# Optimization experiments

Measured on AMD Instinct MI355X. Metric: run time of the kernel, lower is better.

## Reference

```python
import jax, jax.numpy as jnp
import numpy as np
from jax import lax

K = 3
BN_EPS = 1e-5


def knn3(x1, x2):
    """x1: (B,N,3), x2: (B,M,3). Returns squared dists (B,N,K) sorted ascending and idx (B,N,K)."""
    # squared euclidean distances via ||a||^2 + ||b||^2 - 2 a.b
    d = (jnp.sum(x1 * x1, -1)[..., :, None]
         + jnp.sum(x2 * x2, -1)[..., None, :]
         - 2.0 * jnp.einsum('bnc,bmc->bnm', x1, x2))  # (B,N,M)
    neg_d, idx = lax.top_k(-d, K)  # smallest distances first
    return -neg_d, idx


def conv_bn_relu(x, W, b, gamma, beta):
    """1x1 Conv1d + BatchNorm1d (training-mode batch stats) + relu. x: (B,C_in,N)."""
    y = jnp.einsum('oc,bcn->bon', W, x) + b[None, :, None]
    mean = jnp.mean(y, axis=(0, 2), keepdims=True)
    var = jnp.mean((y - mean) ** 2, axis=(0, 2), keepdims=True)  # biased, as torch BN
    y = (y - mean) * lax.rsqrt(var + BN_EPS)
    y = y * gamma[None, :, None] + beta[None, :, None]
    return jax.nn.relu(y)


def setup_inputs() -> dict:
    key = jax.random.key(0)
    ks = jax.random.split(key, 12)
    B, N, M = 8, 8192, 2048
    C2, C1 = 256, 128          # points2 / points1 channels
    Cin = C2 + C1              # MLP input after concat
    H1, H2 = 256, 256          # mlp=[256,256]
    inp = {
        'xyz1': jax.random.normal(ks[0], (B, 3, N), jnp.float32),
        'xyz2': jax.random.normal(ks[1], (B, 3, M), jnp.float32),
        'points1': jax.random.normal(ks[2], (B, C1, N), jnp.float32),
        'points2': jax.random.normal(ks[3], (B, C2, M), jnp.float32),
        'W1': jax.random.normal(ks[4], (H1, Cin), jnp.float32) * (1.0 / np.sqrt(Cin)),
        'b1': jax.random.normal(ks[5], (H1,), jnp.float32) * 0.01,
        'g1': jnp.ones((H1,), jnp.float32),
        'beta1': jnp.zeros((H1,), jnp.float32),
        'W2': jax.random.normal(ks[6], (H2, H1), jnp.float32) * (1.0 / np.sqrt(H1)),
        'b2': jax.random.normal(ks[7], (H2,), jnp.float32) * 0.01,
        'g2': jnp.ones((H2,), jnp.float32),
        'beta2': jnp.zeros((H2,), jnp.float32),
    }
    return inp


def reference(xyz1, xyz2, points1, points2, W1, b1, g1, beta1, W2, b2, g2, beta2):
    # (B,3,N)->(B,N,3)
    x1 = jnp.swapaxes(xyz1, -2, -1)
    x2 = jnp.swapaxes(xyz2, -2, -1)
    p2 = jnp.swapaxes(points2, -2, -1)  # (B,M,C2)

    dist, idx = knn3(x1, x2)  # (B,N,K) squared dists, sorted ascending

    # gather neighbor features: (B,N,K,C2)
    nn_points = jax.vmap(lambda p, i: p[i])(p2, idx)

    # inverse-distance weights (faithful: clamp to 1e-10, then 1/(d+1e-8))
    dist = jnp.maximum(dist, 1e-10)
    dist_recip = 1.0 / (dist + 1e-8)
    weight = dist_recip / jnp.sum(dist_recip, axis=-1, keepdims=True)  # (B,N,K)

    interpolated = jnp.einsum('bnkc,bnk->bcn', nn_points, weight)  # (B,C2,N)

    new_points = jnp.concatenate([interpolated, points1], axis=1)  # (B,C2+C1,N)
    new_points = conv_bn_relu(new_points, W1, b1, g1, beta1)
    new_points = conv_bn_relu(new_points, W2, b2, g2, beta2)
    return new_points
```

## Files before the change

kernel.cpp:

```cpp
#include <hip/hip_runtime.h>
#include <cfloat>
#include <cmath>

#define B_    8
#define N_    8192
#define M_    2048
#define C1_   128
#define C2_   256
#define CIN_  384
#define H_    256
#define BNEPS 1e-5f
#define TJ    64
#define NBLK  ((N_ / TJ) * B_)

typedef __bf16 bf16x8 __attribute__((ext_vector_type(8)));
typedef float  f32x4  __attribute__((ext_vector_type(4)));

__device__ __forceinline__ bool lexless(float d, int m, float dk, int ik) {
    return (d < dk) | ((d == dk) & (m < ik));
}
__device__ __forceinline__ void ins3(float d, int m,
                                     float& d0, int& i0, float& d1, int& i1,
                                     float& d2, int& i2) {
    if (lexless(d, m, d2, i2)) {
        if (lexless(d, m, d1, i1)) {
            d2 = d1; i2 = i1;
            if (lexless(d, m, d0, i0)) { d1 = d0; i1 = i0; d0 = d; i0 = m; }
            else                       { d1 = d;  i1 = m; }
        } else { d2 = d; i2 = m; }
    }
}

__global__ __launch_bounds__(256) void knn_kernel(const float* __restrict__ xyz1,
                                                  const float* __restrict__ xyz2,
                                                  float* __restrict__ wsW,
                                                  int* __restrict__ wsI) {
    __shared__ float4 pts[M_];
    const int b = blockIdx.y;
    const int t = threadIdx.x;
    const int n = blockIdx.x * 64 + (t >> 2);
    const int q = t & 3;

    const float* x2 = xyz2 + (size_t)b * 3 * M_;
    for (int m = t; m < M_; m += 256) {
        float x = x2[m], y = x2[M_ + m], z = x2[2 * M_ + m];
        pts[m] = make_float4(x, y, z, fmaf(z, z, fmaf(y, y, x * x)));
    }
    __syncthreads();

    const float* x1 = xyz1 + (size_t)b * 3 * N_;
    const float px = x1[n], py = x1[N_ + n], pz = x1[2 * N_ + n];
    const float s1 = fmaf(pz, pz, fmaf(py, py, px * px));
    const float ax = -2.0f * px, ay = -2.0f * py, az = -2.0f * pz;

    float d0 = FLT_MAX, d1 = FLT_MAX, d2 = FLT_MAX;
    int   i0 = 0x7fffffff, i1 = 0x7fffffff, i2 = 0x7fffffff;

    const float4* p = pts + q;
    #pragma unroll 8
    for (int it = 0; it < M_ / 4; ++it) {
        const float4 pt = p[it * 4];
        const float d = fmaf(ax, pt.x, fmaf(ay, pt.y, fmaf(az, pt.z, s1 + pt.w)));
        const int m = it * 4 + q;
        const bool c0 = d < d0, c1 = d < d1, c2 = d < d2;
        i2 = c1 ? i1 : (c2 ? m : i2);
        i1 = c0 ? i0 : (c1 ? m : i1);
        i0 = c0 ? m  : i0;
        d2 = __builtin_amdgcn_fmed3f(d, d1, d2);
        d1 = __builtin_amdgcn_fmed3f(d, d0, d1);
        d0 = fminf(d, d0);
    }

    #pragma unroll
    for (int delta = 1; delta <= 2; delta <<= 1) {
        float e0 = __shfl_xor(d0, delta), e1 = __shfl_xor(d1, delta), e2 = __shfl_xor(d2, delta);
        int   j0 = __shfl_xor(i0, delta), j1 = __shfl_xor(i1, delta), j2 = __shfl_xor(i2, delta);
        ins3(e0, j0, d0, i0, d1, i1, d2, i2);
        ins3(e1, j1, d0, i0, d1, i1, d2, i2);
        ins3(e2, j2, d0, i0, d1, i1, d2, i2);
    }

    if (q == 0) {
        const float e0 = fmaxf(d0, 1e-10f) + 1e-8f;
        const float e1 = fmaxf(d1, 1e-10f) + 1e-8f;
        const float e2 = fmaxf(d2, 1e-10f) + 1e-8f;
        const float r0 = 1.0f / e0, r1 = 1.0f / e1, r2 = 1.0f / e2;
        const float sum = r0 + r1 + r2;
        const int BNtot = B_ * N_;
        const int base  = b * N_ + n;
        wsW[base] = r0 / sum;  wsW[BNtot + base] = r1 / sum;  wsW[2 * BNtot + base] = r2 / sum;
        wsI[base] = i0;        wsI[BNtot + base] = i1;        wsI[2 * BNtot + base] = i2;
    }
}

__global__ __launch_bounds__(256) void tp2_kernel(const float* __restrict__ p2,
                                                  __bf16* __restrict__ p2t) {
    __shared__ float tile[32][33];
    const int b  = blockIdx.z;
    const int c0 = blockIdx.x * 32, m0 = blockIdx.y * 32;
    const int tx = threadIdx.x & 31, ty = threadIdx.x >> 5;
    const float* src = p2 + ((size_t)b * C2_ + c0) * M_ + m0;
    #pragma unroll
    for (int r = 0; r < 32; r += 8) tile[ty + r][tx] = src[(size_t)(ty + r) * M_ + tx];
    __syncthreads();
    __bf16* dst = p2t + ((size_t)b * M_ + m0) * C2_ + c0;
    #pragma unroll
    for (int r = 0; r < 32; r += 8) dst[(size_t)(ty + r) * C2_ + tx] = (__bf16)tile[tx][ty + r];
}

__global__ __launch_bounds__(256) void packW_kernel(const float* __restrict__ W,
                                                    unsigned short* __restrict__ Wp,
                                                    int Cin) {
    const int tid = blockIdx.x * 256 + threadIdx.x;
    const int total = (Cin / 32) * 16 * 64;
    if (tid >= total) return;
    const int lane = tid & 63;
    const int ob   = (tid >> 6) & 15;
    const int kc   = tid >> 10;
    const int row  = ob * 16 + (lane & 15);
    const int k0   = kc * 32 + (lane >> 4) * 8;
    const float* src = W + (size_t)row * Cin + k0;
    __bf16* dst = (__bf16*)(Wp + (size_t)tid * 8);
    #pragma unroll
    for (int e = 0; e < 8; ++e) dst[e] = (__bf16)src[e];
}

__global__ __launch_bounds__(256, 2) void gemm1_kernel(const float* __restrict__ points1,
                                                       const __bf16* __restrict__ p2t,
                                                       const bf16x8* __restrict__ W1f,
                                                       const float* __restrict__ bias1,
                                                       const float* __restrict__ wsW,
                                                       const int* __restrict__ wsI,
                                                       __bf16* __restrict__ Y1bf,
                                                       float* __restrict__ partS,
                                                       float* __restrict__ partS2) {
    __shared__ __align__(16) unsigned short Bfrag[2][4][64][8];
    __shared__ float wsh[3][TJ];
    __shared__ int   ish[3][TJ];

    const int b  = blockIdx.y;
    const int n0 = blockIdx.x * TJ;
    const int t  = threadIdx.x;
    const int wave = t >> 6, lane = t & 63;
    const int pid  = b * (N_ / TJ) + blockIdx.x;
    const int BNtot = B_ * N_;

    if (t < 3 * TJ) {
        int k = t / TJ, j = t % TJ;
        wsh[k][j] = wsW[k * BNtot + b * N_ + n0 + j];
        ish[k][j] = wsI[k * BNtot + b * N_ + n0 + j];
    }
    __syncthreads();

    const int j = t >> 2, q = t & 3;
    const float w0 = wsh[0][j], w1 = wsh[1][j], w2 = wsh[2][j];
    const __bf16* r0 = p2t + ((size_t)(b * M_ + ish[0][j])) * C2_;
    const __bf16* r1 = p2t + ((size_t)(b * M_ + ish[1][j])) * C2_;
    const __bf16* r2 = p2t + ((size_t)(b * M_ + ish[2][j])) * C2_;
    const float* p1b = points1 + (size_t)b * C1_ * N_ + n0 + j;
    uint4* dstB[2] = { (uint4*)&Bfrag[0][j >> 4][q * 16 + (j & 15)][0],
                       (uint4*)&Bfrag[1][j >> 4][q * 16 + (j & 15)][0] };

    struct Stage { bf16x8 a, b, c; float f[8]; };
    auto issue = [&](int kc, Stage& S) {
        if (kc < C2_ / 32) {
            const int off = kc * 32 + q * 8;
            S.a = *(const bf16x8*)(r0 + off);
            S.b = *(const bf16x8*)(r1 + off);
            S.c = *(const bf16x8*)(r2 + off);
        } else {
            const int cbase = kc * 32 - C2_ + q * 8;
            #pragma unroll
            for (int e = 0; e < 8; ++e) S.f[e] = p1b[(size_t)(cbase + e) * N_];
        }
    };
    auto packwrite = [&](int kc, const Stage& S, uint4* dst) {
        union { __bf16 h[8]; uint4 u4; } pk;
        if (kc < C2_ / 32) {
            #pragma unroll
            for (int e = 0; e < 8; ++e)
                pk.h[e] = (__bf16)fmaf(w2, (float)S.c[e],
                               fmaf(w1, (float)S.b[e], w0 * (float)S.a[e]));
        } else {
            #pragma unroll
            for (int e = 0; e < 8; ++e) pk.h[e] = (__bf16)S.f[e];
        }
        *dst = pk.u4;
    };

    f32x4 acc[4][4];
    #pragma unroll
    for (int rb = 0; rb < 4; ++rb)
        #pragma unroll
        for (int nb = 0; nb < 4; ++nb) acc[rb][nb] = (f32x4){0.f, 0.f, 0.f, 0.f};

    Stage L;
    bf16x8 af[4], afn[4];
    issue(0, L);
    #pragma unroll
    for (int rb = 0; rb < 4; ++rb)
        af[rb] = W1f[((size_t)0 * 16 + wave * 4 + rb) * 64 + lane];
    packwrite(0, L, dstB[0]);
    __syncthreads();

    #pragma unroll
    for (int kc = 0; kc < CIN_ / 32; ++kc) {
        constexpr int NK = CIN_ / 32;
        Stage Ln;
        if (kc + 1 < NK) {
            issue(kc + 1, Ln);
            #pragma unroll
            for (int rb = 0; rb < 4; ++rb)
                afn[rb] = W1f[((size_t)(kc + 1) * 16 + wave * 4 + rb) * 64 + lane];
        }
        bf16x8 bfr[4];
        #pragma unroll
        for (int nb = 0; nb < 4; ++nb)
            bfr[nb] = *reinterpret_cast<const bf16x8*>(&Bfrag[kc & 1][nb][lane][0]);
        #pragma unroll
        for (int rb = 0; rb < 4; ++rb)
            #pragma unroll
            for (int nb = 0; nb < 4; ++nb)
                acc[rb][nb] = __builtin_amdgcn_mfma_f32_16x16x32_bf16(af[rb], bfr[nb],
                                                                      acc[rb][nb], 0, 0, 0);
        if (kc + 1 < NK) {
            packwrite(kc + 1, Ln, dstB[(kc + 1) & 1]);
            #pragma unroll
            for (int rb = 0; rb < 4; ++rb) af[rb] = afn[rb];
        }
        __syncthreads();
    }

    const int rrow = (lane >> 4) * 4, col = lane & 15;
    #pragma unroll
    for (int rb = 0; rb < 4; ++rb) {
        #pragma unroll
        for (int r = 0; r < 4; ++r) {
            const int o = wave * 64 + rb * 16 + rrow + r;
            const float bv = bias1[o];
            float s = 0.f, s2 = 0.f;
            #pragma unroll
            for (int nb = 0; nb < 4; ++nb) {
                float val = acc[rb][nb][r] + bv;
                Y1bf[((size_t)b * H_ + o) * N_ + n0 + nb * 16 + col] = (__bf16)val;
                s += val;
                s2 = fmaf(val, val, s2);
            }
            #pragma unroll
            for (int delta = 1; delta < 16; delta <<= 1) {
                s  += __shfl_xor(s, delta);
                s2 += __shfl_xor(s2, delta);
            }
            if (col == 0) {
                partS [(size_t)o * NBLK + pid] = s;
                partS2[(size_t)o * NBLK + pid] = s2;
            }
        }
    }
}

__global__ __launch_bounds__(256) void reduce_stats(const float* __restrict__ partS,
                                                    const float* __restrict__ partS2,
                                                    const float* __restrict__ g,
                                                    const float* __restrict__ beta,
                                                    float* __restrict__ sc,
                                                    float* __restrict__ sh) {
    const int c = blockIdx.x;
    const int t = threadIdx.x;
    double s = 0.0, s2 = 0.0;
    #pragma unroll
    for (int i = t; i < NBLK; i += 256) {
        s  += (double)partS [(size_t)c * NBLK + i];
        s2 += (double)partS2[(size_t)c * NBLK + i];
    }
    __shared__ double ls[256], ls2[256];
    ls[t] = s; ls2[t] = s2;
    __syncthreads();
    for (int off = 128; off > 0; off >>= 1) {
        if (t < off) { ls[t] += ls[t + off]; ls2[t] += ls2[t + off]; }
        __syncthreads();
    }
    if (t == 0) {
        const double cnt = (double)B_ * N_;
        double mean = ls[0] / cnt;
        double var  = ls2[0] / cnt - mean * mean;
        float rstd  = (float)(1.0 / sqrt(var + (double)BNEPS));
        float scale = rstd * g[c];
        sc[c] = scale;
        sh[c] = beta[c] - (float)mean * scale;
    }
}

__global__ __launch_bounds__(256, 2) void gemm2_kernel(const bf16x8* __restrict__ W2f,
                                                       const float* __restrict__ bias2,
                                                       const float* __restrict__ sc1,
                                                       const float* __restrict__ sh1,
                                                       __bf16* __restrict__ Ybf,
                                                       float* __restrict__ partS,
                                                       float* __restrict__ partS2) {
    __shared__ __align__(16) unsigned short Bfrag[2][4][64][8];
    __shared__ float scs[H_], shs[H_];

    const int b  = blockIdx.y;
    const int n0 = blockIdx.x * TJ;
    const int t  = threadIdx.x;
    const int wave = t >> 6, lane = t & 63;
    const int pid  = b * (N_ / TJ) + blockIdx.x;

    scs[t] = sc1[t];
    shs[t] = sh1[t];
    __syncthreads();

    const int j = t >> 2, q = t & 3;
    __bf16* Yb = Ybf + (size_t)b * H_ * N_;
    const __bf16* src = Yb + n0 + j;
    uint4* dstB[2] = { (uint4*)&Bfrag[0][j >> 4][q * 16 + (j & 15)][0],
                       (uint4*)&Bfrag[1][j >> 4][q * 16 + (j & 15)][0] };

    auto issue = [&](int kc, float L[8]) {
        #pragma unroll
        for (int e = 0; e < 8; ++e)
            L[e] = (float)src[(size_t)(kc * 32 + q * 8 + e) * N_];
    };
    auto packwrite = [&](int kc, const float L[8], uint4* dst) {
        union { __bf16 h[8]; uint4 u4; } pk;
        #pragma unroll
        for (int e = 0; e < 8; ++e) {
            const int c = kc * 32 + q * 8 + e;
            pk.h[e] = (__bf16)fmaxf(fmaf(L[e], scs[c], shs[c]), 0.0f);
        }
        *dst = pk.u4;
    };

    f32x4 acc[4][4];
    #pragma unroll
    for (int rb = 0; rb < 4; ++rb)
        #pragma unroll
        for (int nb = 0; nb < 4; ++nb) acc[rb][nb] = (f32x4){0.f, 0.f, 0.f, 0.f};

    float L[8];
    bf16x8 af[4], afn[4];
    issue(0, L);
    #pragma unroll
    for (int rb = 0; rb < 4; ++rb)
        af[rb] = W2f[((size_t)0 * 16 + wave * 4 + rb) * 64 + lane];
    packwrite(0, L, dstB[0]);
    __syncthreads();

    #pragma unroll
    for (int kc = 0; kc < H_ / 32; ++kc) {
        constexpr int NK = H_ / 32;
        float Ln[8];
        if (kc + 1 < NK) {
            issue(kc + 1, Ln);
            #pragma unroll
            for (int rb = 0; rb < 4; ++rb)
                afn[rb] = W2f[((size_t)(kc + 1) * 16 + wave * 4 + rb) * 64 + lane];
        }
        bf16x8 bfr[4];
        #pragma unroll
        for (int nb = 0; nb < 4; ++nb)
            bfr[nb] = *reinterpret_cast<const bf16x8*>(&Bfrag[kc & 1][nb][lane][0]);
        #pragma unroll
        for (int rb = 0; rb < 4; ++rb)
            #pragma unroll
            for (int nb = 0; nb < 4; ++nb)
                acc[rb][nb] = __builtin_amdgcn_mfma_f32_16x16x32_bf16(af[rb], bfr[nb],
                                                                      acc[rb][nb], 0, 0, 0);
        if (kc + 1 < NK) {
            packwrite(kc + 1, Ln, dstB[(kc + 1) & 1]);
            #pragma unroll
            for (int rb = 0; rb < 4; ++rb) af[rb] = afn[rb];
        }
        __syncthreads();
    }

    const int rrow = (lane >> 4) * 4, col = lane & 15;
    #pragma unroll
    for (int rb = 0; rb < 4; ++rb) {
        #pragma unroll
        for (int r = 0; r < 4; ++r) {
            const int o = wave * 64 + rb * 16 + rrow + r;
            const float bv = bias2[o];
            float s = 0.f, s2 = 0.f;
            #pragma unroll
            for (int nb = 0; nb < 4; ++nb) {
                float val = acc[rb][nb][r] + bv;
                Yb[(size_t)o * N_ + n0 + nb * 16 + col] = (__bf16)val;
                s += val;
                s2 = fmaf(val, val, s2);
            }
            #pragma unroll
            for (int delta = 1; delta < 16; delta <<= 1) {
                s  += __shfl_xor(s, delta);
                s2 += __shfl_xor(s2, delta);
            }
            if (col == 0) {
                partS [(size_t)o * NBLK + pid] = s;
                partS2[(size_t)o * NBLK + pid] = s2;
            }
        }
    }
}

__global__ __launch_bounds__(256) void bnrelu_kernel(const __bf16* __restrict__ Ybf,
                                                     float* __restrict__ out,
                                                     const float* __restrict__ sc,
                                                     const float* __restrict__ sh) {
    const size_t total8 = (size_t)B_ * H_ * N_ / 8;
    const size_t stride = (size_t)gridDim.x * 256;
    for (size_t i = (size_t)blockIdx.x * 256 + threadIdx.x; i < total8; i += stride) {
        bf16x8 v = ((const bf16x8*)Ybf)[i];
        const int c = (int)((i / (N_ / 8)) % H_);
        const float a = sc[c], d = sh[c];
        float4 lo, hi;
        lo.x = fmaxf(fmaf((float)v[0], a, d), 0.f);
        lo.y = fmaxf(fmaf((float)v[1], a, d), 0.f);
        lo.z = fmaxf(fmaf((float)v[2], a, d), 0.f);
        lo.w = fmaxf(fmaf((float)v[3], a, d), 0.f);
        hi.x = fmaxf(fmaf((float)v[4], a, d), 0.f);
        hi.y = fmaxf(fmaf((float)v[5], a, d), 0.f);
        hi.z = fmaxf(fmaf((float)v[6], a, d), 0.f);
        hi.w = fmaxf(fmaf((float)v[7], a, d), 0.f);
        ((float4*)out)[i * 2]     = lo;
        ((float4*)out)[i * 2 + 1] = hi;
    }
}

extern "C" void kernel_launch(void* const* d_in, const int* in_sizes, int n_in,
                              void* d_out, int out_size, void* d_ws, size_t ws_size,
                              hipStream_t stream) {
    const float* xyz1    = (const float*)d_in[0];
    const float* xyz2    = (const float*)d_in[1];
    const float* points1 = (const float*)d_in[2];
    const float* points2 = (const float*)d_in[3];
    const float* W1      = (const float*)d_in[4];
    const float* b1      = (const float*)d_in[5];
    const float* g1      = (const float*)d_in[6];
    const float* beta1   = (const float*)d_in[7];
    const float* W2      = (const float*)d_in[8];
    const float* b2      = (const float*)d_in[9];
    const float* g2      = (const float*)d_in[10];
    const float* beta2   = (const float*)d_in[11];
    float* out = (float*)d_out;

    const int BNtot = B_ * N_;
    char* ws = (char*)d_ws;
    size_t off = 0;
    float* wsW = (float*)(ws + off);  off += (size_t)3 * BNtot * 4;
    int*   wsI = (int*)(ws + off);    off += (size_t)3 * BNtot * 4;
    float* sc1 = (float*)(ws + off);  off += H_ * 4;
    float* sh1 = (float*)(ws + off);  off += H_ * 4;
    float* sc2 = (float*)(ws + off);  off += H_ * 4;
    float* sh2 = (float*)(ws + off);  off += H_ * 4;
    __bf16* p2t = (__bf16*)(ws + off); off += (size_t)B_ * M_ * C2_ * 2;
    unsigned short* W1p = (unsigned short*)(ws + off); off += (size_t)H_ * CIN_ * 2;
    unsigned short* W2p = (unsigned short*)(ws + off); off += (size_t)H_ * H_ * 2;
    float* partS  = (float*)(ws + off); off += (size_t)H_ * NBLK * 4;
    float* partS2 = (float*)(ws + off); off += (size_t)H_ * NBLK * 4;
    __bf16* ybf   = (__bf16*)(ws + off); off += (size_t)B_ * H_ * N_ * 2;

    knn_kernel<<<dim3(N_ / 64, B_), 256, 0, stream>>>(xyz1, xyz2, wsW, wsI);
    tp2_kernel<<<dim3(C2_ / 32, M_ / 32, B_), 256, 0, stream>>>(points2, p2t);
    packW_kernel<<<(CIN_ / 32 * 16 * 64 + 255) / 256, 256, 0, stream>>>(W1, W1p, CIN_);
    packW_kernel<<<(H_ / 32 * 16 * 64 + 255) / 256, 256, 0, stream>>>(W2, W2p, H_);

    gemm1_kernel<<<dim3(N_ / TJ, B_), 256, 0, stream>>>(points1, p2t, (const bf16x8*)W1p,
                                                        b1, wsW, wsI, ybf, partS, partS2);
    reduce_stats<<<H_, 256, 0, stream>>>(partS, partS2, g1, beta1, sc1, sh1);
    gemm2_kernel<<<dim3(N_ / TJ, B_), 256, 0, stream>>>((const bf16x8*)W2p, b2, sc1, sh1,
                                                        ybf, partS, partS2);
    reduce_stats<<<H_, 256, 0, stream>>>(partS, partS2, g2, beta2, sc2, sh2);
    bnrelu_kernel<<<4096, 256, 0, stream>>>(ybf, out, sc2, sh2);
}
```

Measured before the change: 158.5 us.

## Shrink gemm1 tile to 32 points with 2 waves and triple-buffered prefetch

Gemm1 now processes 32 points per block with 128 threads. Each wave covers 128 output rows, and the grid doubles so there are more blocks. Gather loads are issued two k-chunks ahead, using three shared-memory B buffers and double-buffered A fragments, to hide the latency of the kNN gather. The cost is more blocks, more partial-stat entries for reduce_stats (now taking nblk as a parameter), and higher register pressure from 8x2 accumulators plus two in-flight stages.

```diff
diff --git a/kernel.cpp b/kernel.cpp
--- a/kernel.cpp
+++ b/kernel.cpp
@@ -11,7 +11,9 @@
 #define H_    256
 #define BNEPS 1e-5f
 #define TJ    64
-#define NBLK  ((N_ / TJ) * B_)
+#define TJ1   32
+#define NBLK1 ((N_ / TJ1) * B_)
+#define NBLK2 ((N_ / TJ)  * B_)
 
 typedef __bf16 bf16x8 __attribute__((ext_vector_type(8)));
 typedef float  f32x4  __attribute__((ext_vector_type(4)));
@@ -125,7 +127,7 @@
     for (int e = 0; e < 8; ++e) dst[e] = (__bf16)src[e];
 }
 
-__global__ __launch_bounds__(256, 2) void gemm1_kernel(const float* __restrict__ points1,
+__global__ __launch_bounds__(128, 2) void gemm1_kernel(const float* __restrict__ points1,
                                                        const __bf16* __restrict__ p2t,
                                                        const bf16x8* __restrict__ W1f,
                                                        const float* __restrict__ bias1,
@@ -134,19 +136,19 @@
                                                        __bf16* __restrict__ Y1bf,
                                                        float* __restrict__ partS,
                                                        float* __restrict__ partS2) {
-    __shared__ __align__(16) unsigned short Bfrag[2][4][64][8];
-    __shared__ float wsh[3][TJ];
-    __shared__ int   ish[3][TJ];
+    __shared__ __align__(16) unsigned short Bfrag[3][2][64][8];
+    __shared__ float wsh[3][TJ1];
+    __shared__ int   ish[3][TJ1];
 
     const int b  = blockIdx.y;
-    const int n0 = blockIdx.x * TJ;
+    const int n0 = blockIdx.x * TJ1;
     const int t  = threadIdx.x;
     const int wave = t >> 6, lane = t & 63;
-    const int pid  = b * (N_ / TJ) + blockIdx.x;
+    const int pid  = b * (N_ / TJ1) + blockIdx.x;
     const int BNtot = B_ * N_;
 
-    if (t < 3 * TJ) {
-        int k = t / TJ, j = t % TJ;
+    if (t < 3 * TJ1) {
+        int k = t >> 5, j = t & 31;
         wsh[k][j] = wsW[k * BNtot + b * N_ + n0 + j];
         ish[k][j] = wsI[k * BNtot + b * N_ + n0 + j];
     }
@@ -158,8 +160,9 @@
     const __bf16* r1 = p2t + ((size_t)(b * M_ + ish[1][j])) * C2_;
     const __bf16* r2 = p2t + ((size_t)(b * M_ + ish[2][j])) * C2_;
     const float* p1b = points1 + (size_t)b * C1_ * N_ + n0 + j;
-    uint4* dstB[2] = { (uint4*)&Bfrag[0][j >> 4][q * 16 + (j & 15)][0],
-                       (uint4*)&Bfrag[1][j >> 4][q * 16 + (j & 15)][0] };
+    uint4* dstB[3] = { (uint4*)&Bfrag[0][j >> 4][q * 16 + (j & 15)][0],
+                       (uint4*)&Bfrag[1][j >> 4][q * 16 + (j & 15)][0],
+                       (uint4*)&Bfrag[2][j >> 4][q * 16 + (j & 15)][0] };
 
     struct Stage { bf16x8 a, b, c; float f[8]; };
     auto issue = [&](int kc, Stage& S) {
@@ -188,59 +191,55 @@
         *dst = pk.u4;
     };
 
-    f32x4 acc[4][4];
-    #pragma unroll
-    for (int rb = 0; rb < 4; ++rb)
-        #pragma unroll
-        for (int nb = 0; nb < 4; ++nb) acc[rb][nb] = (f32x4){0.f, 0.f, 0.f, 0.f};
-
-    Stage L;
-    bf16x8 af[4], afn[4];
-    issue(0, L);
-    #pragma unroll
-    for (int rb = 0; rb < 4; ++rb)
-        af[rb] = W1f[((size_t)0 * 16 + wave * 4 + rb) * 64 + lane];
-    packwrite(0, L, dstB[0]);
-    __syncthreads();
-
-    #pragma unroll
-    for (int kc = 0; kc < CIN_ / 32; ++kc) {
-        constexpr int NK = CIN_ / 32;
-        Stage Ln;
+    constexpr int NK = CIN_ / 32;
+    f32x4 acc[8][2];
+    #pragma unroll
+    for (int rb = 0; rb < 8; ++rb) {
+        acc[rb][0] = (f32x4){0.f, 0.f, 0.f, 0.f};
+        acc[rb][1] = (f32x4){0.f, 0.f, 0.f, 0.f};
+    }
+
+    Stage SA, SB;
+    bf16x8 afA[8], afB[8];
+    issue(0, SA);
+    issue(1, SB);
+    #pragma unroll
+    for (int rb = 0; rb < 8; ++rb)
+        afA[rb] = W1f[((size_t)0 * 16 + wave * 8 + rb) * 64 + lane];
+    packwrite(0, SA, dstB[0]);
+    __syncthreads();
+
+    #pragma unroll
+    for (int kc = 0; kc < NK; ++kc) {
+        if (kc + 2 < NK) issue(kc + 2, (kc & 1) ? SB : SA);
+        bf16x8 (&afn)[8] = ((kc + 1) & 1) ? afB : afA;
         if (kc + 1 < NK) {
-            issue(kc + 1, Ln);
-            #pragma unroll
-            for (int rb = 0; rb < 4; ++rb)
-                afn[rb] = W1f[((size_t)(kc + 1) * 16 + wave * 4 + rb) * 64 + lane];
-        }
-        bf16x8 bfr[4];
-        #pragma unroll
-        for (int nb = 0; nb < 4; ++nb)
-            bfr[nb] = *reinterpret_cast<const bf16x8*>(&Bfrag[kc & 1][nb][lane][0]);
-        #pragma unroll
-        for (int rb = 0; rb < 4; ++rb)
-            #pragma unroll
-            for (int nb = 0; nb < 4; ++nb)
-                acc[rb][nb] = __builtin_amdgcn_mfma_f32_16x16x32_bf16(af[rb], bfr[nb],
-                                                                      acc[rb][nb], 0, 0, 0);
-        if (kc + 1 < NK) {
-            packwrite(kc + 1, Ln, dstB[(kc + 1) & 1]);
-            #pragma unroll
-            for (int rb = 0; rb < 4; ++rb) af[rb] = afn[rb];
-        }
+            #pragma unroll
+            for (int rb = 0; rb < 8; ++rb)
+                afn[rb] = W1f[((size_t)(kc + 1) * 16 + wave * 8 + rb) * 64 + lane];
+        }
+        bf16x8 (&afc)[8] = (kc & 1) ? afB : afA;
+        const bf16x8 bfr0 = *reinterpret_cast<const bf16x8*>(&Bfrag[kc % 3][0][lane][0]);
+        const bf16x8 bfr1 = *reinterpret_cast<const bf16x8*>(&Bfrag[kc % 3][1][lane][0]);
+        #pragma unroll
+        for (int rb = 0; rb < 8; ++rb) {
+            acc[rb][0] = __builtin_amdgcn_mfma_f32_16x16x32_bf16(afc[rb], bfr0, acc[rb][0], 0, 0, 0);
+            acc[rb][1] = __builtin_amdgcn_mfma_f32_16x16x32_bf16(afc[rb], bfr1, acc[rb][1], 0, 0, 0);
+        }
+        if (kc + 1 < NK) packwrite(kc + 1, (kc & 1) ? SA : SB, dstB[(kc + 1) % 3]);
         __syncthreads();
     }
 
     const int rrow = (lane >> 4) * 4, col = lane & 15;
     #pragma unroll
-    for (int rb = 0; rb < 4; ++rb) {
+    for (int rb = 0; rb < 8; ++rb) {
         #pragma unroll
         for (int r = 0; r < 4; ++r) {
-            const int o = wave * 64 + rb * 16 + rrow + r;
+            const int o = wave * 128 + rb * 16 + rrow + r;
             const float bv = bias1[o];
             float s = 0.f, s2 = 0.f;
             #pragma unroll
-            for (int nb = 0; nb < 4; ++nb) {
+            for (int nb = 0; nb < 2; ++nb) {
                 float val = acc[rb][nb][r] + bv;
                 Y1bf[((size_t)b * H_ + o) * N_ + n0 + nb * 16 + col] = (__bf16)val;
                 s += val;
@@ -252,8 +251,8 @@
                 s2 += __shfl_xor(s2, delta);
             }
             if (col == 0) {
-                partS [(size_t)o * NBLK + pid] = s;
-                partS2[(size_t)o * NBLK + pid] = s2;
+                partS [(size_t)o * NBLK1 + pid] = s;
+                partS2[(size_t)o * NBLK1 + pid] = s2;
             }
         }
     }
@@ -264,14 +263,14 @@
                                                     const float* __restrict__ g,
                                                     const float* __restrict__ beta,
                                                     float* __restrict__ sc,
-                                                    float* __restrict__ sh) {
+                                                    float* __restrict__ sh,
+                                                    int nblk) {
     const int c = blockIdx.x;
     const int t = threadIdx.x;
     double s = 0.0, s2 = 0.0;
-    #pragma unroll
-    for (int i = t; i < NBLK; i += 256) {
-        s  += (double)partS [(size_t)c * NBLK + i];
-        s2 += (double)partS2[(size_t)c * NBLK + i];
+    for (int i = t; i < nblk; i += 256) {
+        s  += (double)partS [(size_t)c * nblk + i];
+        s2 += (double)partS2[(size_t)c * nblk + i];
     }
     __shared__ double ls[256], ls2[256];
     ls[t] = s; ls2[t] = s2;
@@ -396,8 +395,8 @@
                 s2 += __shfl_xor(s2, delta);
             }
             if (col == 0) {
-                partS [(size_t)o * NBLK + pid] = s;
-                partS2[(size_t)o * NBLK + pid] = s2;
+                partS [(size_t)o * NBLK2 + pid] = s;
+                partS2[(size_t)o * NBLK2 + pid] = s2;
             }
         }
     }
@@ -456,8 +455,8 @@
     __bf16* p2t = (__bf16*)(ws + off); off += (size_t)B_ * M_ * C2_ * 2;
     unsigned short* W1p = (unsigned short*)(ws + off); off += (size_t)H_ * CIN_ * 2;
     unsigned short* W2p = (unsigned short*)(ws + off); off += (size_t)H_ * H_ * 2;
-    float* partS  = (float*)(ws + off); off += (size_t)H_ * NBLK * 4;
-    float* partS2 = (float*)(ws + off); off += (size_t)H_ * NBLK * 4;
+    float* partS  = (float*)(ws + off); off += (size_t)H_ * NBLK1 * 4;
+    float* partS2 = (float*)(ws + off); off += (size_t)H_ * NBLK1 * 4;
     __bf16* ybf   = (__bf16*)(ws + off); off += (size_t)B_ * H_ * N_ * 2;
 
     knn_kernel<<<dim3(N_ / 64, B_), 256, 0, stream>>>(xyz1, xyz2, wsW, wsI);
@@ -465,11 +464,11 @@
     packW_kernel<<<(CIN_ / 32 * 16 * 64 + 255) / 256, 256, 0, stream>>>(W1, W1p, CIN_);
     packW_kernel<<<(H_ / 32 * 16 * 64 + 255) / 256, 256, 0, stream>>>(W2, W2p, H_);
 
-    gemm1_kernel<<<dim3(N_ / TJ, B_), 256, 0, stream>>>(points1, p2t, (const bf16x8*)W1p,
-                                                        b1, wsW, wsI, ybf, partS, partS2);
-    reduce_stats<<<H_, 256, 0, stream>>>(partS, partS2, g1, beta1, sc1, sh1);
+    gemm1_kernel<<<dim3(N_ / TJ1, B_), 128, 0, stream>>>(points1, p2t, (const bf16x8*)W1p,
+                                                         b1, wsW, wsI, ybf, partS, partS2);
+    reduce_stats<<<H_, 256, 0, stream>>>(partS, partS2, g1, beta1, sc1, sh1, NBLK1);
     gemm2_kernel<<<dim3(N_ / TJ, B_), 256, 0, stream>>>((const bf16x8*)W2p, b2, sc1, sh1,
                                                         ybf, partS, partS2);
-    reduce_stats<<<H_, 256, 0, stream>>>(partS, partS2, g2, beta2, sc2, sh2);
+    reduce_stats<<<H_, 256, 0, stream>>>(partS, partS2, g2, beta2, sc2, sh2, NBLK2);
     bnrelu_kernel<<<4096, 256, 0, stream>>>(ybf, out, sc2, sh2);
 }
```

New measurement: 170.8 us. 1.08x slower.

## Fuse KNN search into gemm1 kernel with shared-memory union

Applied to the files above, without the earlier changes.

Moves the 3-NN search and inverse-distance weight computation into the first GEMM kernel, so weights and indices go straight to shared memory rather than through a global workspace. This removes one kernel launch and the global write and read of the weight/index arrays. The point cloud buffer (32KB) shares LDS with the B-fragment buffer through a union, which raises the kernel's LDS footprint. The KNN phase's ALU-heavy loop now runs inside the GEMM kernel and may limit occupancy or serialize with the MFMA phase.

```diff
diff --git a/kernel.cpp b/kernel.cpp
--- a/kernel.cpp
+++ b/kernel.cpp
@@ -28,68 +28,6 @@
             if (lexless(d, m, d0, i0)) { d1 = d0; i1 = i0; d0 = d; i0 = m; }
             else                       { d1 = d;  i1 = m; }
         } else { d2 = d; i2 = m; }
-    }
-}
-
-__global__ __launch_bounds__(256) void knn_kernel(const float* __restrict__ xyz1,
-                                                  const float* __restrict__ xyz2,
-                                                  float* __restrict__ wsW,
-                                                  int* __restrict__ wsI) {
-    __shared__ float4 pts[M_];
-    const int b = blockIdx.y;
-    const int t = threadIdx.x;
-    const int n = blockIdx.x * 64 + (t >> 2);
-    const int q = t & 3;
-
-    const float* x2 = xyz2 + (size_t)b * 3 * M_;
-    for (int m = t; m < M_; m += 256) {
-        float x = x2[m], y = x2[M_ + m], z = x2[2 * M_ + m];
-        pts[m] = make_float4(x, y, z, fmaf(z, z, fmaf(y, y, x * x)));
-    }
-    __syncthreads();
-
-    const float* x1 = xyz1 + (size_t)b * 3 * N_;
-    const float px = x1[n], py = x1[N_ + n], pz = x1[2 * N_ + n];
-    const float s1 = fmaf(pz, pz, fmaf(py, py, px * px));
-    const float ax = -2.0f * px, ay = -2.0f * py, az = -2.0f * pz;
-
-    float d0 = FLT_MAX, d1 = FLT_MAX, d2 = FLT_MAX;
-    int   i0 = 0x7fffffff, i1 = 0x7fffffff, i2 = 0x7fffffff;
-
-    const float4* p = pts + q;
-    #pragma unroll 8
-    for (int it = 0; it < M_ / 4; ++it) {
-        const float4 pt = p[it * 4];
-        const float d = fmaf(ax, pt.x, fmaf(ay, pt.y, fmaf(az, pt.z, s1 + pt.w)));
-        const int m = it * 4 + q;
-        const bool c0 = d < d0, c1 = d < d1, c2 = d < d2;
-        i2 = c1 ? i1 : (c2 ? m : i2);
-        i1 = c0 ? i0 : (c1 ? m : i1);
-        i0 = c0 ? m  : i0;
-        d2 = __builtin_amdgcn_fmed3f(d, d1, d2);
-        d1 = __builtin_amdgcn_fmed3f(d, d0, d1);
-        d0 = fminf(d, d0);
-    }
-
-    #pragma unroll
-    for (int delta = 1; delta <= 2; delta <<= 1) {
-        float e0 = __shfl_xor(d0, delta), e1 = __shfl_xor(d1, delta), e2 = __shfl_xor(d2, delta);
-        int   j0 = __shfl_xor(i0, delta), j1 = __shfl_xor(i1, delta), j2 = __shfl_xor(i2, delta);
-        ins3(e0, j0, d0, i0, d1, i1, d2, i2);
-        ins3(e1, j1, d0, i0, d1, i1, d2, i2);
-        ins3(e2, j2, d0, i0, d1, i1, d2, i2);
-    }
-
-    if (q == 0) {
-        const float e0 = fmaxf(d0, 1e-10f) + 1e-8f;
-        const float e1 = fmaxf(d1, 1e-10f) + 1e-8f;
-        const float e2 = fmaxf(d2, 1e-10f) + 1e-8f;
-        const float r0 = 1.0f / e0, r1 = 1.0f / e1, r2 = 1.0f / e2;
-        const float sum = r0 + r1 + r2;
-        const int BNtot = B_ * N_;
-        const int base  = b * N_ + n;
-        wsW[base] = r0 / sum;  wsW[BNtot + base] = r1 / sum;  wsW[2 * BNtot + base] = r2 / sum;
-        wsI[base] = i0;        wsI[BNtot + base] = i1;        wsI[2 * BNtot + base] = i2;
     }
 }
 
@@ -125,16 +63,20 @@
     for (int e = 0; e < 8; ++e) dst[e] = (__bf16)src[e];
 }
 
-__global__ __launch_bounds__(256, 2) void gemm1_kernel(const float* __restrict__ points1,
-                                                       const __bf16* __restrict__ p2t,
-                                                       const bf16x8* __restrict__ W1f,
-                                                       const float* __restrict__ bias1,
-                                                       const float* __restrict__ wsW,
-                                                       const int* __restrict__ wsI,
-                                                       __bf16* __restrict__ Y1bf,
-                                                       float* __restrict__ partS,
-                                                       float* __restrict__ partS2) {
-    __shared__ __align__(16) unsigned short Bfrag[2][4][64][8];
+__global__ __launch_bounds__(256, 2) void knn_gemm1_kernel(const float* __restrict__ xyz1,
+                                                           const float* __restrict__ xyz2,
+                                                           const float* __restrict__ points1,
+                                                           const __bf16* __restrict__ p2t,
+                                                           const bf16x8* __restrict__ W1f,
+                                                           const float* __restrict__ bias1,
+                                                           __bf16* __restrict__ Y1bf,
+                                                           float* __restrict__ partS,
+                                                           float* __restrict__ partS2) {
+    union SharedU {
+        float4 pts[M_];
+        unsigned short Bfrag[2][4][64][8];
+    };
+    __shared__ SharedU su;
     __shared__ float wsh[3][TJ];
     __shared__ int   ish[3][TJ];
 
@@ -143,23 +85,68 @@
     const int t  = threadIdx.x;
     const int wave = t >> 6, lane = t & 63;
     const int pid  = b * (N_ / TJ) + blockIdx.x;
-    const int BNtot = B_ * N_;
-
-    if (t < 3 * TJ) {
-        int k = t / TJ, j = t % TJ;
-        wsh[k][j] = wsW[k * BNtot + b * N_ + n0 + j];
-        ish[k][j] = wsI[k * BNtot + b * N_ + n0 + j];
-    }
-    __syncthreads();
-
     const int j = t >> 2, q = t & 3;
+
+    {
+        const float* x2 = xyz2 + (size_t)b * 3 * M_;
+        for (int m = t; m < M_; m += 256) {
+            float x = x2[m], y = x2[M_ + m], z = x2[2 * M_ + m];
+            su.pts[m] = make_float4(x, y, z, fmaf(z, z, fmaf(y, y, x * x)));
+        }
+        __syncthreads();
+
+        const int n = n0 + j;
+        const float* x1 = xyz1 + (size_t)b * 3 * N_;
+        const float px = x1[n], py = x1[N_ + n], pz = x1[2 * N_ + n];
+        const float s1 = fmaf(pz, pz, fmaf(py, py, px * px));
+        const float ax = -2.0f * px, ay = -2.0f * py, az = -2.0f * pz;
+
+        float d0 = FLT_MAX, d1 = FLT_MAX, d2 = FLT_MAX;
+        int   i0 = 0x7fffffff, i1 = 0x7fffffff, i2 = 0x7fffffff;
+
+        const float4* p = su.pts + q;
+        #pragma unroll 8
+        for (int it = 0; it < M_ / 4; ++it) {
+            const float4 pt = p[it * 4];
+            const float d = fmaf(ax, pt.x, fmaf(ay, pt.y, fmaf(az, pt.z, s1 + pt.w)));
+            const int m = it * 4 + q;
+            const bool c0 = d < d0, c1 = d < d1, c2 = d < d2;
+            i2 = c1 ? i1 : (c2 ? m : i2);
+            i1 = c0 ? i0 : (c1 ? m : i1);
+            i0 = c0 ? m  : i0;
+            d2 = __builtin_amdgcn_fmed3f(d, d1, d2);
+            d1 = __builtin_amdgcn_fmed3f(d, d0, d1);
+            d0 = fminf(d, d0);
+        }
+
+        #pragma unroll
+        for (int delta = 1; delta <= 2; delta <<= 1) {
+            float e0 = __shfl_xor(d0, delta), e1 = __shfl_xor(d1, delta), e2 = __shfl_xor(d2, delta);
+            int   j0 = __shfl_xor(i0, delta), j1 = __shfl_xor(i1, delta), j2 = __shfl_xor(i2, delta);
+            ins3(e0, j0, d0, i0, d1, i1, d2, i2);
+            ins3(e1, j1, d0, i0, d1, i1, d2, i2);
+            ins3(e2, j2, d0, i0, d1, i1, d2, i2);
+        }
+
+        if (q == 0) {
+            const float e0 = fmaxf(d0, 1e-10f) + 1e-8f;
+            const float e1 = fmaxf(d1, 1e-10f) + 1e-8f;
+            const float e2 = fmaxf(d2, 1e-10f) + 1e-8f;
+            const float r0 = 1.0f / e0, r1 = 1.0f / e1, r2 = 1.0f / e2;
+            const float sum = r0 + r1 + r2;
+            wsh[0][j] = r0 / sum;  wsh[1][j] = r1 / sum;  wsh[2][j] = r2 / sum;
+            ish[0][j] = i0;        ish[1][j] = i1;        ish[2][j] = i2;
+        }
+        __syncthreads();
+    }
+
     const float w0 = wsh[0][j], w1 = wsh[1][j], w2 = wsh[2][j];
     const __bf16* r0 = p2t + ((size_t)(b * M_ + ish[0][j])) * C2_;
     const __bf16* r1 = p2t + ((size_t)(b * M_ + ish[1][j])) * C2_;
     const __bf16* r2 = p2t + ((size_t)(b * M_ + ish[2][j])) * C2_;
     const float* p1b = points1 + (size_t)b * C1_ * N_ + n0 + j;
-    uint4* dstB[2] = { (uint4*)&Bfrag[0][j >> 4][q * 16 + (j & 15)][0],
-                       (uint4*)&Bfrag[1][j >> 4][q * 16 + (j & 15)][0] };
+    uint4* dstB[2] = { (uint4*)&su.Bfrag[0][j >> 4][q * 16 + (j & 15)][0],
+                       (uint4*)&su.Bfrag[1][j >> 4][q * 16 + (j & 15)][0] };
 
     struct Stage { bf16x8 a, b, c; float f[8]; };
     auto issue = [&](int kc, Stage& S) {
@@ -216,7 +203,7 @@
         bf16x8 bfr[4];
         #pragma unroll
         for (int nb = 0; nb < 4; ++nb)
-            bfr[nb] = *reinterpret_cast<const bf16x8*>(&Bfrag[kc & 1][nb][lane][0]);
+            bfr[nb] = *reinterpret_cast<const bf16x8*>(&su.Bfrag[kc & 1][nb][lane][0]);
         #pragma unroll
         for (int rb = 0; rb < 4; ++rb)
             #pragma unroll
@@ -444,11 +431,8 @@
     const float* beta2   = (const float*)d_in[11];
     float* out = (float*)d_out;
 
-    const int BNtot = B_ * N_;
     char* ws = (char*)d_ws;
     size_t off = 0;
-    float* wsW = (float*)(ws + off);  off += (size_t)3 * BNtot * 4;
-    int*   wsI = (int*)(ws + off);    off += (size_t)3 * BNtot * 4;
     float* sc1 = (float*)(ws + off);  off += H_ * 4;
     float* sh1 = (float*)(ws + off);  off += H_ * 4;
     float* sc2 = (float*)(ws + off);  off += H_ * 4;
@@ -460,13 +444,13 @@
     float* partS2 = (float*)(ws + off); off += (size_t)H_ * NBLK * 4;
     __bf16* ybf   = (__bf16*)(ws + off); off += (size_t)B_ * H_ * N_ * 2;
 
-    knn_kernel<<<dim3(N_ / 64, B_), 256, 0, stream>>>(xyz1, xyz2, wsW, wsI);
     tp2_kernel<<<dim3(C2_ / 32, M_ / 32, B_), 256, 0, stream>>>(points2, p2t);
     packW_kernel<<<(CIN_ / 32 * 16 * 64 + 255) / 256, 256, 0, stream>>>(W1, W1p, CIN_);
     packW_kernel<<<(H_ / 32 * 16 * 64 + 255) / 256, 256, 0, stream>>>(W2, W2p, H_);
 
-    gemm1_kernel<<<dim3(N_ / TJ, B_), 256, 0, stream>>>(points1, p2t, (const bf16x8*)W1p,
-                                                        b1, wsW, wsI, ybf, partS, partS2);
+    knn_gemm1_kernel<<<dim3(N_ / TJ, B_), 256, 0, stream>>>(xyz1, xyz2, points1, p2t,
+                                                            (const bf16x8*)W1p, b1,
+                                                            ybf, partS, partS2);
     reduce_stats<<<H_, 256, 0, stream>>>(partS, partS2, g1, beta1, sc1, sh1);
     gemm2_kernel<<<dim3(N_ / TJ, B_), 256, 0, stream>>>((const bf16x8*)W2p, b2, sc1, sh1,
                                                         ybf, partS, partS2);
```

Measured after the change: 147.2 us, median of 2. 7.2% less time.
